# Kernel optimization log

Measured on AMD Instinct MI355X. Metric: run time of the kernel, lower is better.

## Reference

```python
import jax, jax.numpy as jnp
import numpy as np

N_NODES = 100000
N_EDGES = 1000000
IN_FEATS = 64
HID = 128
NUM_CLASSES = 10


def setup_inputs() -> dict:
    key = jax.random.key(0)
    ks = jax.random.split(key, 8)
    x = jax.random.normal(ks[0], (N_NODES, IN_FEATS), dtype=jnp.float32)
    edge_index = jax.random.randint(ks[1], (2, N_EDGES), 0, N_NODES, dtype=jnp.int64)
    # Glorot-style init scale for weights
    def w(k, fan_in, fan_out):
        s = (2.0 / (fan_in + fan_out)) ** 0.5
        return jax.random.normal(k, (fan_in, fan_out), dtype=jnp.float32) * s
    return {
        "x": x,
        "edge_index": edge_index,
        "W1": w(ks[2], IN_FEATS, HID),
        "b1": jnp.zeros((HID,), dtype=jnp.float32),
        "W2": w(ks[3], HID, HID),
        "b2": jnp.zeros((HID,), dtype=jnp.float32),
        "Wl": w(ks[4], HID, NUM_CLASSES),
        "bl": jnp.zeros((NUM_CLASSES,), dtype=jnp.float32),
    }


def _gcn_conv(x, src, dst, norm, W, b, num_nodes):
    # PyG GCNConv: h = x W, then out_i = sum_{j->i} norm_ij * h_j + b
    h = x @ W  # [N, out]
    msgs = h[src] * norm[:, None]  # gather + scale  [E+N, out]
    out = jax.ops.segment_sum(msgs, dst, num_segments=num_nodes)
    return out + b


def reference(x, edge_index, W1, b1, W2, b2, Wl, bl):
    N = x.shape[0]
    loops = jnp.arange(N, dtype=edge_index.dtype)
    src = jnp.concatenate([edge_index[0], loops])  # source nodes (messages from)
    dst = jnp.concatenate([edge_index[1], loops])  # target nodes (aggregate at)
    # symmetric normalization: deg over targets (includes self-loops)
    deg = jax.ops.segment_sum(jnp.ones(dst.shape, dtype=x.dtype), dst, num_segments=N)
    dinv = jnp.where(deg > 0, jax.lax.rsqrt(deg), 0.0)
    norm = dinv[src] * dinv[dst]  # [E+N]

    h = jax.nn.relu(_gcn_conv(x, src, dst, norm, W1, b1, N))
    h = jax.nn.relu(_gcn_conv(h, src, dst, norm, W2, b2, N))
    return jax.nn.log_softmax(h @ Wl + bl, axis=1)
```

## Files before the change

### kernel.cpp

```cpp
#include <hip/hip_runtime.h>
#include <hip/hip_fp16.h>
#include <math.h>

#define NUM_CLASSES 10

#define BSH 9
#define BSZ 512
#define BCAP 6144

typedef _Float16 half8  __attribute__((ext_vector_type(8)));
typedef _Float16 half4t __attribute__((ext_vector_type(4)));
typedef float    floatx4 __attribute__((ext_vector_type(4)));

__global__ __launch_bounds__(256) void prep_kernel(const float* __restrict__ W1,
                                                   const float* __restrict__ W2,
                                                   _Float16* __restrict__ W1t,
                                                   _Float16* __restrict__ W2t,
                                                   int* __restrict__ fill, int nbuck) {
    const int b = blockIdx.x, tid = threadIdx.x;
    if (b == 0 && tid < nbuck) fill[tid] = 0;
    if (b < 32) {
        int i = b * 256 + tid;
        int k = i >> 7, c = i & 127;
        W1t[c * 72 + k] = (_Float16)W1[i];
    } else {
        int i = (b - 32) * 256 + tid;
        int k = i >> 7, c = i & 127;
        W2t[c * 136 + k] = (_Float16)W2[i];
    }
}

__global__ __launch_bounds__(256) void csr_p1_kernel(const int* __restrict__ src,
                                                     const int* __restrict__ dst,
                                                     int* __restrict__ bucket_fill,
                                                     uint2* __restrict__ pairs, int E) {
    __shared__ int hist[256], base[256], cur[256];
    const int tid = threadIdx.x;
    hist[tid] = 0;
    cur[tid] = 0;
    __syncthreads();
    const int bb = blockIdx.x * 2048;
    int s[8], d[8], bk[8];
    int cnt = 0;
#pragma unroll
    for (int i = 0; i < 8; ++i) {
        int idx = bb + i * 256 + tid;
        if (idx < E) {
            s[i] = src[idx];
            d[i] = dst[idx];
            bk[i] = d[i] >> BSH;
            atomicAdd(&hist[bk[i]], 1);
            cnt = i + 1;
        }
    }
    __syncthreads();
    if (hist[tid] > 0) base[tid] = atomicAdd(&bucket_fill[tid], hist[tid]);
    __syncthreads();
#pragma unroll
    for (int i = 0; i < 8; ++i) {
        if (i < cnt) {
            int b = bk[i];
            int r = atomicAdd(&cur[b], 1) + base[b];
            if (r < BCAP) pairs[(size_t)b * BCAP + r] = make_uint2((unsigned)s[i], (unsigned)d[i]);
        }
    }
}

__global__ __launch_bounds__(256) void csr_p2_kernel(const int* __restrict__ bucket_fill,
                                                     const uint2* __restrict__ pairs,
                                                     int* __restrict__ rowstart,
                                                     float* __restrict__ dinv,
                                                     int* __restrict__ csr_src,
                                                     int N, int nbuck) {
    __shared__ int cnt[BSZ], excl[BSZ], cur[BSZ];
    __shared__ int s1[256];
    const int tid = threadIdx.x;
    const int b = blockIdx.x;
    const int node0 = b << BSH;
    const int nodes_b = min(BSZ, N - node0);

    cnt[tid] = 0; cnt[tid + 256] = 0;
    cur[tid] = 0; cur[tid + 256] = 0;
    s1[tid] = (tid < b) ? bucket_fill[tid] : 0;
    __syncthreads();
    for (int off = 128; off > 0; off >>= 1) {
        if (tid < off) s1[tid] += s1[tid + off];
        __syncthreads();
    }
    const int bbase = s1[0];
    const int ne = bucket_fill[b];
    __syncthreads();

    const uint2* bp = pairs + (size_t)b * BCAP;
    for (int i = tid; i < ne; i += 256)
        atomicAdd(&cnt[(int)bp[i].y - node0], 1);
    __syncthreads();
    int c0 = cnt[2 * tid], c1 = cnt[2 * tid + 1];
    s1[tid] = c0 + c1;
    __syncthreads();
    for (int off = 1; off < 256; off <<= 1) {
        int t = (tid >= off) ? s1[tid - off] : 0;
        __syncthreads();
        s1[tid] += t;
        __syncthreads();
    }
    int ex = s1[tid] - (c0 + c1);
    excl[2 * tid] = ex;
    excl[2 * tid + 1] = ex + c0;
    __syncthreads();
    for (int i = tid; i < nodes_b; i += 256) {
        rowstart[node0 + i] = bbase + excl[i];
        dinv[node0 + i] = rsqrtf((float)cnt[i] + 1.0f);
    }
    if (b == nbuck - 1 && tid == 0) rowstart[N] = bbase + ne;
    for (int i = tid; i < ne; i += 256) {
        uint2 p = bp[i];
        int d = (int)p.y - node0;
        int r = atomicAdd(&cur[d], 1);
        csr_src[bbase + excl[d] + r] = (int)p.x;
    }
}

__global__ __launch_bounds__(256) void prescale_h_kernel(const float* __restrict__ x,
                                                         const float* __restrict__ dinv,
                                                         __half2* __restrict__ xs, int n2) {
    int gid = blockIdx.x * 256 + threadIdx.x;
    if (gid < n2) {
        float d = dinv[gid >> 5];
        float2 v = ((const float2*)x)[gid];
        xs[gid] = __floats2half2_rn(v.x * d, v.y * d);
    }
}

template <int F>
__global__ __launch_bounds__(256) void gather_h_kernel(const __half2* __restrict__ hs,
                                                       const float* __restrict__ dinv,
                                                       const int* __restrict__ rowstart,
                                                       const int* __restrict__ csr_src,
                                                       __half2* __restrict__ out, int N) {
    constexpr int F2 = F / 2;
    int node = (blockIdx.x * 256 + threadIdx.x) >> 6;
    int lane = threadIdx.x & 63;
    if (node >= N) return;
    int f2 = lane & (F2 - 1);

    int beg = rowstart[node];
    int end = rowstart[node + 1];
    int deg = end - beg;

    float2 self = __half22float2(hs[(size_t)node * F2 + f2]);
    int lim = deg < 64 ? deg : 64;
    int myidx = (lane < lim) ? csr_src[beg + lane] : node;
    int itersUp = (lim + 3) & ~3;
    float comp = (float)(1 - (itersUp - lim));
    float2 acc;
    acc.x = self.x * comp;
    acc.y = self.y * comp;

    for (int j = 0; j < itersUp; j += 4) {
        int s0 = __shfl(myidx, j);
        int s1 = __shfl(myidx, j + 1);
        int s2 = __shfl(myidx, j + 2);
        int s3 = __shfl(myidx, j + 3);
        float2 v0 = __half22float2(hs[(size_t)s0 * F2 + f2]);
        float2 v1 = __half22float2(hs[(size_t)s1 * F2 + f2]);
        float2 v2 = __half22float2(hs[(size_t)s2 * F2 + f2]);
        float2 v3 = __half22float2(hs[(size_t)s3 * F2 + f2]);
        acc.x += (v0.x + v1.x) + (v2.x + v3.x);
        acc.y += (v0.y + v1.y) + (v2.y + v3.y);
    }
    for (int j = beg + 64; j < end; ++j) {
        int s = csr_src[j];
        float2 v = __half22float2(hs[(size_t)s * F2 + f2]);
        acc.x += v.x;
        acc.y += v.y;
    }
    if (F == 128 || lane < 32) {
        float d = dinv[node];
        out[(size_t)node * F2 + f2] = __floats2half2_rn(d * acc.x, d * acc.y);
    }
}

template <int K, bool SCALE_OUT>
__global__ __launch_bounds__(256) void gemm_mfma_kernel(const _Float16* __restrict__ In,
                                                        const _Float16* __restrict__ Wt,
                                                        const float* __restrict__ bias,
                                                        const float* __restrict__ dinv,
                                                        _Float16* __restrict__ Out, int N) {
    constexpr int KP = K + 8;
    constexpr int NC = K / 32;
    __shared__ _Float16 Wl[128 * KP];
    __shared__ float bias_s[128];
    const int tid = threadIdx.x;

    for (int i = tid; i < (128 * KP) / 8; i += 256)
        ((floatx4*)Wl)[i] = ((const floatx4*)Wt)[i];
    if (tid < 128) bias_s[tid] = bias[tid];
    __syncthreads();

    const int lane = tid & 63;
    const int wave = tid >> 6;
    const int q = lane >> 4;
    const int l15 = lane & 15;

#pragma unroll
    for (int iter = 0; iter < 2; ++iter) {
        int myrow = blockIdx.x * 128 + iter * 64 + wave * 16 + l15;
        int r = myrow < N ? myrow : N - 1;
        half8 xf[NC];
#pragma unroll
        for (int c = 0; c < NC; ++c)
            xf[c] = *(const half8*)(In + (size_t)r * K + c * 32 + q * 8);
        floatx4 acc[8];
#pragma unroll
        for (int t = 0; t < 8; ++t) acc[t] = (floatx4){0.f, 0.f, 0.f, 0.f};
#pragma unroll
        for (int c = 0; c < NC; ++c) {
#pragma unroll
            for (int t = 0; t < 8; ++t) {
                half8 wf = *(const half8*)(Wl + (t * 16 + l15) * KP + c * 32 + q * 8);
                acc[t] = __builtin_amdgcn_mfma_f32_16x16x32_f16(wf, xf[c], acc[t], 0, 0, 0);
            }
        }
        if (myrow < N) {
            float sc = SCALE_OUT ? dinv[myrow] : 1.0f;
#pragma unroll
            for (int t = 0; t < 8; ++t) {
                int c0 = t * 16 + q * 4;
                floatx4 bv = *(const floatx4*)&bias_s[c0];
                half4t h;
#pragma unroll
                for (int j = 0; j < 4; ++j)
                    h[j] = (_Float16)(sc * fmaxf(acc[t][j] + bv[j], 0.0f));
                *(half4t*)(Out + (size_t)myrow * 128 + c0) = h;
            }
        }
    }
}

__global__ __launch_bounds__(256) void final_h_kernel(const __half* __restrict__ act,
                                                      const float* __restrict__ Wl,
                                                      const float* __restrict__ bl,
                                                      float* __restrict__ out, int N) {
    __shared__ __align__(16) __half rows[256 * 128];
    const int tid = threadIdx.x;
    const int row0 = blockIdx.x * 256;

#pragma unroll
    for (int i = 0; i < 16; ++i) {
        int g = i * 256 + tid;
        int r = g >> 4, c = g & 15;
        int grow = row0 + r;
        float4 v = make_float4(0.f, 0.f, 0.f, 0.f);
        if (grow < N) v = *(const float4*)(act + (size_t)grow * 128 + c * 8);
        int pc = c ^ (r & 15);
        *(float4*)&rows[r * 128 + pc * 8] = v;
    }
    __syncthreads();

    const int r = tid;
    float acc[NUM_CLASSES];
#pragma unroll
    for (int cls = 0; cls < NUM_CLASSES; ++cls) acc[cls] = bl[cls];

    for (int c = 0; c < 16; ++c) {
        int pc = c ^ (r & 15);
        float4 raw = *(const float4*)&rows[r * 128 + pc * 8];
        __half2 hp[4];
        *(float4*)hp = raw;
        float2 f[4];
#pragma unroll
        for (int j = 0; j < 4; ++j) f[j] = __half22float2(hp[j]);
#pragma unroll
        for (int j = 0; j < 4; ++j) {
            int k0 = c * 8 + 2 * j;
#pragma unroll
            for (int cls = 0; cls < NUM_CLASSES; ++cls) {
                acc[cls] += f[j].x * Wl[k0 * NUM_CLASSES + cls]
                          + f[j].y * Wl[(k0 + 1) * NUM_CLASSES + cls];
            }
        }
    }

    float m = acc[0];
#pragma unroll
    for (int cls = 1; cls < NUM_CLASSES; ++cls) m = fmaxf(m, acc[cls]);
    float s = 0.0f;
#pragma unroll
    for (int cls = 0; cls < NUM_CLASSES; ++cls) s += expf(acc[cls] - m);
    float lse = m + logf(s);

    int grow = row0 + r;
    if (grow < N) {
        float2* op = (float2*)(out + (size_t)grow * NUM_CLASSES);
#pragma unroll
        for (int j = 0; j < 5; ++j)
            op[j] = make_float2(acc[2 * j] - lse, acc[2 * j + 1] - lse);
    }
}

extern "C" void kernel_launch(void* const* d_in, const int* in_sizes, int n_in,
                              void* d_out, int out_size, void* d_ws, size_t ws_size,
                              hipStream_t stream) {
    const float* x  = (const float*)d_in[0];
    const int*   ei = (const int*)d_in[1];
    const float* W1 = (const float*)d_in[2];
    const float* b1 = (const float*)d_in[3];
    const float* W2 = (const float*)d_in[4];
    const float* b2 = (const float*)d_in[5];
    const float* Wl = (const float*)d_in[6];
    const float* bl = (const float*)d_in[7];
    float* out = (float*)d_out;

    const int N = in_sizes[0] / 64;
    const int E = in_sizes[1] / 2;
    const int* src = ei;
    const int* dst = ei + E;
    const int nbuck = (N + BSZ - 1) >> BSH;

    char* ws = (char*)d_ws;
    int*      bucket_fill = (int*)(ws + 0);
    int*      rowstart    = (int*)(ws + 4096);
    float*    dinv        = (float*)(ws + 524288);
    _Float16* W1t         = (_Float16*)(ws + 1048576);
    _Float16* W2t         = (_Float16*)(ws + 1069056);
    uint2*    pairs       = (uint2*)(ws + 2097152);
    int*      csr_src     = (int*)(ws + 12582912);
    char*     region1     = ws + 16777216;
    char*     region2     = ws + 68157440;
    __half2*  xs_h = (__half2*)region1;
    __half2*  g1h  = (__half2*)(region1 + 13631488);
    __half2*  g2h  = (__half2*)region1;
    __half2*  a1_h = (__half2*)region2;
    _Float16* a2_h = (_Float16*)region2;

    const int P1B = (E + 2047) / 2048;
    const int GB  = (N + 127) / 128;
    const int WVB = (N + 3) / 4;
    const int PHB = (N * 32 + 255) / 256;
    const int FB  = (N + 255) / 256;

    prep_kernel<<<96, 256, 0, stream>>>(W1, W2, W1t, W2t, bucket_fill, nbuck);
    csr_p1_kernel<<<P1B, 256, 0, stream>>>(src, dst, bucket_fill, pairs, E);
    csr_p2_kernel<<<nbuck, 256, 0, stream>>>(bucket_fill, pairs, rowstart, dinv, csr_src, N, nbuck);

    prescale_h_kernel<<<PHB, 256, 0, stream>>>(x, dinv, xs_h, N * 32);
    gather_h_kernel<64><<<WVB, 256, 0, stream>>>(xs_h, dinv, rowstart, csr_src, g1h, N);
    gemm_mfma_kernel<64, true><<<GB, 256, 0, stream>>>((const _Float16*)g1h, W1t, b1, dinv,
                                                       (_Float16*)a1_h, N);

    gather_h_kernel<128><<<WVB, 256, 0, stream>>>(a1_h, dinv, rowstart, csr_src, g2h, N);
    gemm_mfma_kernel<128, false><<<GB, 256, 0, stream>>>((const _Float16*)g2h, W2t, b2, dinv,
                                                         a2_h, N);

    final_h_kernel<<<FB, 256, 0, stream>>>((const __half*)a2_h, Wl, bl, out, N);
}
```

Measured before the change: 252.5 us.

## Fuse prescale into CSR build, pack edge pairs, fuse final layer via MFMA

Packs (src, local dst) into one 32-bit word to halve bucketed pair traffic. Folds the feature prescale into the CSR second pass, which removes one kernel launch. Fuses the second GEMM with the classifier and log-softmax using MFMA on a padded 16-class weight tile, so the layer-2 activations are no longer written to and read back from global memory. Raises the gather unroll from 4 to 8, which adds padding work for low-degree nodes. The packing assumes node ids fit in 23 bits.

```diff
diff --git a/kernel.cpp b/kernel.cpp
--- a/kernel.cpp
+++ b/kernel.cpp
@@ -14,8 +14,10 @@
 
 __global__ __launch_bounds__(256) void prep_kernel(const float* __restrict__ W1,
                                                    const float* __restrict__ W2,
+                                                   const float* __restrict__ Wlc,
                                                    _Float16* __restrict__ W1t,
                                                    _Float16* __restrict__ W2t,
+                                                   _Float16* __restrict__ Wct,
                                                    int* __restrict__ fill, int nbuck) {
     const int b = blockIdx.x, tid = threadIdx.x;
     if (b == 0 && tid < nbuck) fill[tid] = 0;
@@ -23,32 +25,39 @@
         int i = b * 256 + tid;
         int k = i >> 7, c = i & 127;
         W1t[c * 72 + k] = (_Float16)W1[i];
-    } else {
+    } else if (b < 96) {
         int i = (b - 32) * 256 + tid;
         int k = i >> 7, c = i & 127;
         W2t[c * 136 + k] = (_Float16)W2[i];
+    } else {
+        for (int i = tid; i < 16 * 136; i += 256) {
+            int c = i / 136, k = i - c * 136;
+            float v = (c < NUM_CLASSES && k < 128) ? Wlc[k * NUM_CLASSES + c] : 0.0f;
+            Wct[i] = (_Float16)v;
+        }
     }
 }
 
 __global__ __launch_bounds__(256) void csr_p1_kernel(const int* __restrict__ src,
                                                      const int* __restrict__ dst,
                                                      int* __restrict__ bucket_fill,
-                                                     uint2* __restrict__ pairs, int E) {
+                                                     unsigned* __restrict__ pairs, int E) {
     __shared__ int hist[256], base[256], cur[256];
     const int tid = threadIdx.x;
     hist[tid] = 0;
     cur[tid] = 0;
     __syncthreads();
     const int bb = blockIdx.x * 2048;
-    int s[8], d[8], bk[8];
+    unsigned pk[8];
+    int bk[8];
     int cnt = 0;
 #pragma unroll
     for (int i = 0; i < 8; ++i) {
         int idx = bb + i * 256 + tid;
         if (idx < E) {
-            s[i] = src[idx];
-            d[i] = dst[idx];
-            bk[i] = d[i] >> BSH;
+            int s = src[idx], d = dst[idx];
+            bk[i] = d >> BSH;
+            pk[i] = ((unsigned)s << BSH) | (unsigned)(d & (BSZ - 1));
             atomicAdd(&hist[bk[i]], 1);
             cnt = i + 1;
         }
@@ -61,16 +70,18 @@
         if (i < cnt) {
             int b = bk[i];
             int r = atomicAdd(&cur[b], 1) + base[b];
-            if (r < BCAP) pairs[(size_t)b * BCAP + r] = make_uint2((unsigned)s[i], (unsigned)d[i]);
+            if (r < BCAP) pairs[(size_t)b * BCAP + r] = pk[i];
         }
     }
 }
 
 __global__ __launch_bounds__(256) void csr_p2_kernel(const int* __restrict__ bucket_fill,
-                                                     const uint2* __restrict__ pairs,
+                                                     const unsigned* __restrict__ pairs,
+                                                     const float* __restrict__ x,
                                                      int* __restrict__ rowstart,
                                                      float* __restrict__ dinv,
                                                      int* __restrict__ csr_src,
+                                                     __half2* __restrict__ xs_h,
                                                      int N, int nbuck) {
     __shared__ int cnt[BSZ], excl[BSZ], cur[BSZ];
     __shared__ int s1[256];
@@ -91,9 +102,9 @@
     const int ne = bucket_fill[b];
     __syncthreads();
 
-    const uint2* bp = pairs + (size_t)b * BCAP;
+    const unsigned* bp = pairs + (size_t)b * BCAP;
     for (int i = tid; i < ne; i += 256)
-        atomicAdd(&cnt[(int)bp[i].y - node0], 1);
+        atomicAdd(&cnt[bp[i] & (BSZ - 1)], 1);
     __syncthreads();
     int c0 = cnt[2 * tid], c1 = cnt[2 * tid + 1];
     s1[tid] = c0 + c1;
@@ -113,22 +124,17 @@
         dinv[node0 + i] = rsqrtf((float)cnt[i] + 1.0f);
     }
     if (b == nbuck - 1 && tid == 0) rowstart[N] = bbase + ne;
+    for (int i = tid; i < nodes_b * 32; i += 256) {
+        int ln = i >> 5;
+        float d = rsqrtf((float)cnt[ln] + 1.0f);
+        float2 v = ((const float2*)x)[(size_t)node0 * 32 + i];
+        xs_h[(size_t)node0 * 32 + i] = __floats2half2_rn(v.x * d, v.y * d);
+    }
     for (int i = tid; i < ne; i += 256) {
-        uint2 p = bp[i];
-        int d = (int)p.y - node0;
+        unsigned p = bp[i];
+        int d = (int)(p & (BSZ - 1));
         int r = atomicAdd(&cur[d], 1);
-        csr_src[bbase + excl[d] + r] = (int)p.x;
-    }
-}
-
-__global__ __launch_bounds__(256) void prescale_h_kernel(const float* __restrict__ x,
-                                                         const float* __restrict__ dinv,
-                                                         __half2* __restrict__ xs, int n2) {
-    int gid = blockIdx.x * 256 + threadIdx.x;
-    if (gid < n2) {
-        float d = dinv[gid >> 5];
-        float2 v = ((const float2*)x)[gid];
-        xs[gid] = __floats2half2_rn(v.x * d, v.y * d);
+        csr_src[bbase + excl[d] + r] = (int)(p >> BSH);
     }
 }
 
@@ -151,23 +157,21 @@
     float2 self = __half22float2(hs[(size_t)node * F2 + f2]);
     int lim = deg < 64 ? deg : 64;
     int myidx = (lane < lim) ? csr_src[beg + lane] : node;
-    int itersUp = (lim + 3) & ~3;
+    int itersUp = (lim + 7) & ~7;
     float comp = (float)(1 - (itersUp - lim));
     float2 acc;
     acc.x = self.x * comp;
     acc.y = self.y * comp;
 
-    for (int j = 0; j < itersUp; j += 4) {
-        int s0 = __shfl(myidx, j);
-        int s1 = __shfl(myidx, j + 1);
-        int s2 = __shfl(myidx, j + 2);
-        int s3 = __shfl(myidx, j + 3);
-        float2 v0 = __half22float2(hs[(size_t)s0 * F2 + f2]);
-        float2 v1 = __half22float2(hs[(size_t)s1 * F2 + f2]);
-        float2 v2 = __half22float2(hs[(size_t)s2 * F2 + f2]);
-        float2 v3 = __half22float2(hs[(size_t)s3 * F2 + f2]);
-        acc.x += (v0.x + v1.x) + (v2.x + v3.x);
-        acc.y += (v0.y + v1.y) + (v2.y + v3.y);
+    for (int j = 0; j < itersUp; j += 8) {
+        int s[8];
+#pragma unroll
+        for (int u = 0; u < 8; ++u) s[u] = __shfl(myidx, j + u);
+        float2 v[8];
+#pragma unroll
+        for (int u = 0; u < 8; ++u) v[u] = __half22float2(hs[(size_t)s[u] * F2 + f2]);
+#pragma unroll
+        for (int u = 0; u < 8; ++u) { acc.x += v[u].x; acc.y += v[u].y; }
     }
     for (int j = beg + 64; j < end; ++j) {
         int s = csr_src[j];
@@ -238,64 +242,96 @@
     }
 }
 
-__global__ __launch_bounds__(256) void final_h_kernel(const __half* __restrict__ act,
-                                                      const float* __restrict__ Wl,
-                                                      const float* __restrict__ bl,
-                                                      float* __restrict__ out, int N) {
-    __shared__ __align__(16) __half rows[256 * 128];
+__global__ __launch_bounds__(256) void gemm_final_kernel(const _Float16* __restrict__ In,
+                                                         const _Float16* __restrict__ Wt,
+                                                         const float* __restrict__ bias,
+                                                         const _Float16* __restrict__ Wct,
+                                                         const float* __restrict__ bl,
+                                                         float* __restrict__ out, int N) {
+    constexpr int K = 128, KP = 136, NC = 4;
+    __shared__ _Float16 Wl[128 * KP];
+    __shared__ _Float16 Wc[16 * KP];
+    __shared__ float bias_s[128];
+    __shared__ float bl_s[16];
+    __shared__ _Float16 act_s[4][16 * KP];
     const int tid = threadIdx.x;
-    const int row0 = blockIdx.x * 256;
-
-#pragma unroll
-    for (int i = 0; i < 16; ++i) {
-        int g = i * 256 + tid;
-        int r = g >> 4, c = g & 15;
-        int grow = row0 + r;
-        float4 v = make_float4(0.f, 0.f, 0.f, 0.f);
-        if (grow < N) v = *(const float4*)(act + (size_t)grow * 128 + c * 8);
-        int pc = c ^ (r & 15);
-        *(float4*)&rows[r * 128 + pc * 8] = v;
-    }
-    __syncthreads();
-
-    const int r = tid;
-    float acc[NUM_CLASSES];
-#pragma unroll
-    for (int cls = 0; cls < NUM_CLASSES; ++cls) acc[cls] = bl[cls];
-
-    for (int c = 0; c < 16; ++c) {
-        int pc = c ^ (r & 15);
-        float4 raw = *(const float4*)&rows[r * 128 + pc * 8];
-        __half2 hp[4];
-        *(float4*)hp = raw;
-        float2 f[4];
-#pragma unroll
-        for (int j = 0; j < 4; ++j) f[j] = __half22float2(hp[j]);
-#pragma unroll
-        for (int j = 0; j < 4; ++j) {
-            int k0 = c * 8 + 2 * j;
-#pragma unroll
-            for (int cls = 0; cls < NUM_CLASSES; ++cls) {
-                acc[cls] += f[j].x * Wl[k0 * NUM_CLASSES + cls]
-                          + f[j].y * Wl[(k0 + 1) * NUM_CLASSES + cls];
+
+    for (int i = tid; i < (128 * KP) / 8; i += 256)
+        ((floatx4*)Wl)[i] = ((const floatx4*)Wt)[i];
+    for (int i = tid; i < (16 * KP) / 8; i += 256)
+        ((floatx4*)Wc)[i] = ((const floatx4*)Wct)[i];
+    if (tid < 128) bias_s[tid] = bias[tid];
+    if (tid < 16) bl_s[tid] = (tid < NUM_CLASSES) ? bl[tid] : -1e30f;
+    __syncthreads();
+
+    const int lane = tid & 63;
+    const int wave = tid >> 6;
+    const int q = lane >> 4;
+    const int l15 = lane & 15;
+    _Float16* As = act_s[wave];
+
+    half8 wcf[NC];
+#pragma unroll
+    for (int c = 0; c < NC; ++c)
+        wcf[c] = *(const half8*)(Wc + l15 * KP + c * 32 + q * 8);
+    float myclsb[4];
+#pragma unroll
+    for (int reg = 0; reg < 4; ++reg) myclsb[reg] = bl_s[q * 4 + reg];
+
+#pragma unroll
+    for (int iter = 0; iter < 2; ++iter) {
+        int rowbase = blockIdx.x * 128 + iter * 64 + wave * 16;
+        int myrow = rowbase + l15;
+        int r = myrow < N ? myrow : N - 1;
+        half8 xf[NC];
+#pragma unroll
+        for (int c = 0; c < NC; ++c)
+            xf[c] = *(const half8*)(In + (size_t)r * K + c * 32 + q * 8);
+        floatx4 acc[8];
+#pragma unroll
+        for (int t = 0; t < 8; ++t) acc[t] = (floatx4){0.f, 0.f, 0.f, 0.f};
+#pragma unroll
+        for (int c = 0; c < NC; ++c) {
+#pragma unroll
+            for (int t = 0; t < 8; ++t) {
+                half8 wf = *(const half8*)(Wl + (t * 16 + l15) * KP + c * 32 + q * 8);
+                acc[t] = __builtin_amdgcn_mfma_f32_16x16x32_f16(wf, xf[c], acc[t], 0, 0, 0);
             }
         }
-    }
-
-    float m = acc[0];
-#pragma unroll
-    for (int cls = 1; cls < NUM_CLASSES; ++cls) m = fmaxf(m, acc[cls]);
-    float s = 0.0f;
-#pragma unroll
-    for (int cls = 0; cls < NUM_CLASSES; ++cls) s += expf(acc[cls] - m);
-    float lse = m + logf(s);
-
-    int grow = row0 + r;
-    if (grow < N) {
-        float2* op = (float2*)(out + (size_t)grow * NUM_CLASSES);
-#pragma unroll
-        for (int j = 0; j < 5; ++j)
-            op[j] = make_float2(acc[2 * j] - lse, acc[2 * j + 1] - lse);
+#pragma unroll
+        for (int t = 0; t < 8; ++t) {
+            int c0 = t * 16 + q * 4;
+            floatx4 bv = *(const floatx4*)&bias_s[c0];
+            half4t h;
+#pragma unroll
+            for (int j = 0; j < 4; ++j)
+                h[j] = (_Float16)fmaxf(acc[t][j] + bv[j], 0.0f);
+            *(half4t*)&As[l15 * KP + c0] = h;
+        }
+        floatx4 lg = (floatx4){0.f, 0.f, 0.f, 0.f};
+#pragma unroll
+        for (int c = 0; c < NC; ++c) {
+            half8 af = *(const half8*)(As + l15 * KP + c * 32 + q * 8);
+            lg = __builtin_amdgcn_mfma_f32_16x16x32_f16(wcf[c], af, lg, 0, 0, 0);
+        }
+        if (myrow < N) {
+            float v[4];
+#pragma unroll
+            for (int reg = 0; reg < 4; ++reg) v[reg] = lg[reg] + myclsb[reg];
+            float mx = fmaxf(fmaxf(v[0], v[1]), fmaxf(v[2], v[3]));
+            mx = fmaxf(mx, __shfl_xor(mx, 16));
+            mx = fmaxf(mx, __shfl_xor(mx, 32));
+            float sm = expf(v[0] - mx) + expf(v[1] - mx) + expf(v[2] - mx) + expf(v[3] - mx);
+            sm += __shfl_xor(sm, 16);
+            sm += __shfl_xor(sm, 32);
+            float lse = mx + logf(sm);
+#pragma unroll
+            for (int reg = 0; reg < 4; ++reg) {
+                int cls = q * 4 + reg;
+                if (cls < NUM_CLASSES)
+                    out[(size_t)myrow * NUM_CLASSES + cls] = v[reg] - lse;
+            }
+        }
     }
 }
 
@@ -308,7 +344,7 @@
     const float* b1 = (const float*)d_in[3];
     const float* W2 = (const float*)d_in[4];
     const float* b2 = (const float*)d_in[5];
-    const float* Wl = (const float*)d_in[6];
+    const float* Wlc = (const float*)d_in[6];
     const float* bl = (const float*)d_in[7];
     float* out = (float*)d_out;
 
@@ -324,7 +360,8 @@
     float*    dinv        = (float*)(ws + 524288);
     _Float16* W1t         = (_Float16*)(ws + 1048576);
     _Float16* W2t         = (_Float16*)(ws + 1069056);
-    uint2*    pairs       = (uint2*)(ws + 2097152);
+    _Float16* Wct         = (_Float16*)(ws + 1103872);
+    unsigned* pairs       = (unsigned*)(ws + 2097152);
     int*      csr_src     = (int*)(ws + 12582912);
     char*     region1     = ws + 16777216;
     char*     region2     = ws + 68157440;
@@ -332,26 +369,20 @@
     __half2*  g1h  = (__half2*)(region1 + 13631488);
     __half2*  g2h  = (__half2*)region1;
     __half2*  a1_h = (__half2*)region2;
-    _Float16* a2_h = (_Float16*)region2;
 
     const int P1B = (E + 2047) / 2048;
     const int GB  = (N + 127) / 128;
     const int WVB = (N + 3) / 4;
-    const int PHB = (N * 32 + 255) / 256;
-    const int FB  = (N + 255) / 256;
-
-    prep_kernel<<<96, 256, 0, stream>>>(W1, W2, W1t, W2t, bucket_fill, nbuck);
+
+    prep_kernel<<<97, 256, 0, stream>>>(W1, W2, Wlc, W1t, W2t, Wct, bucket_fill, nbuck);
     csr_p1_kernel<<<P1B, 256, 0, stream>>>(src, dst, bucket_fill, pairs, E);
-    csr_p2_kernel<<<nbuck, 256, 0, stream>>>(bucket_fill, pairs, rowstart, dinv, csr_src, N, nbuck);
-
-    prescale_h_kernel<<<PHB, 256, 0, stream>>>(x, dinv, xs_h, N * 32);
+    csr_p2_kernel<<<nbuck, 256, 0, stream>>>(bucket_fill, pairs, x, rowstart, dinv,
+                                             csr_src, xs_h, N, nbuck);
+
     gather_h_kernel<64><<<WVB, 256, 0, stream>>>(xs_h, dinv, rowstart, csr_src, g1h, N);
     gemm_mfma_kernel<64, true><<<GB, 256, 0, stream>>>((const _Float16*)g1h, W1t, b1, dinv,
                                                        (_Float16*)a1_h, N);
 
     gather_h_kernel<128><<<WVB, 256, 0, stream>>>(a1_h, dinv, rowstart, csr_src, g2h, N);
-    gemm_mfma_kernel<128, false><<<GB, 256, 0, stream>>>((const _Float16*)g2h, W2t, b2, dinv,
-                                                         a2_h, N);
-
-    final_h_kernel<<<FB, 256, 0, stream>>>((const __half*)a2_h, Wl, bl, out, N);
-}
+    gemm_final_kernel<<<GB, 256, 0, stream>>>((const _Float16*)g2h, W2t, b2, Wct, bl, out, N);
+}
```

Measured after the change: 250.9 us. About the same (-0.6%).
